# Performance work log

Measured on AMD Instinct MI355X. Metric: run time of the kernel, lower is better.

The kernel has to match this reference:

```python
import jax, jax.numpy as jnp
import numpy as np

N = 128          # number of nodes (particles)
NR = N * (N - 1) # number of directed edges, receiver-major order
B = 128          # batch
C = 16           # channel dim


def setup_inputs() -> dict:
    key = jax.random.key(0)
    x = jax.random.normal(key, (B, NR, C), dtype=jnp.float32)
    # assign_matrices enumerates (r, s) pairs receiver-major, so edge i has
    # receiver i // (N-1); Rr2 is the one-hot indicator of this mapping.
    receivers = jnp.arange(NR, dtype=jnp.int32) // (N - 1)
    return {"x": x, "receivers": receivers}


def reference(x, receivers):
    # exp of edge scores
    e = jnp.exp(x)  # [B, Nr, C]
    # tensordot(exp, Rr2, axes=[1,1]) == segment-sum over edges grouped by receiver
    seg = jax.ops.segment_sum(e.transpose(1, 0, 2), receivers, num_segments=N)  # [N, B, C]
    # tensordot(exp_sum, Rr2, axes=1) == gather each edge's receiver sum back to edges
    denom = seg[receivers]                 # [Nr, B, C]
    denom = denom.transpose(1, 2, 0)       # [B, C, Nr]
    # NOTE: the original divides the raw inputs (not exp) by the summed exp
    return x.transpose(0, 2, 1) / denom    # [B, C, Nr]
```

## Files before the change

kernel.cpp:

```cpp
#include <hip/hip_runtime.h>

#define NN   128
#define NE   127
#define CH   16
#define NRE  (NN * NE)
#define STR  128

__global__ __launch_bounds__(256) void attn2_kernel(const float* __restrict__ x,
                                                    float* __restrict__ out) {
    __shared__ float tile[4][CH * STR];

    const int t   = threadIdx.x & 63;
    const int w   = threadIdx.x >> 6;
    const int seg = (blockIdx.x << 2) | w;
    const int b   = seg >> 7;
    const int r   = seg & (NN - 1);

    float* T = tile[w];

    const float4* xseg = (const float4*)(x + (size_t)seg * NE * CH);

    float4 v[8];
    #pragma unroll
    for (int it = 0; it < 8; ++it) {
        int f = t + (it << 6);
        v[it] = xseg[f < 508 ? f : 507];
    }

    const int p  = (t & 3) << 2;
    const int er = t >> 2;
    float a0 = 0.f, a1 = 0.f, a2 = 0.f, a3 = 0.f;
    #pragma unroll
    for (int it = 0; it < 8; ++it) {
        int f = t + (it << 6);
        if (f < 508) {
            int edge = er + (it << 4);
            T[(p + 0) * STR + edge] = v[it].x;
            T[(p + 1) * STR + edge] = v[it].y;
            T[(p + 2) * STR + edge] = v[it].z;
            T[(p + 3) * STR + edge] = v[it].w;
            a0 += __expf(v[it].x); a1 += __expf(v[it].y);
            a2 += __expf(v[it].z); a3 += __expf(v[it].w);
        }
    }

    #pragma unroll
    for (int m = 4; m <= 32; m <<= 1) {
        a0 += __shfl_xor(a0, m, 64);
        a1 += __shfl_xor(a1, m, 64);
        a2 += __shfl_xor(a2, m, 64);
        a3 += __shfl_xor(a3, m, 64);
    }
    if (t < 4) {
        T[(p + 0) * STR + NE] = 1.0f / a0;
        T[(p + 1) * STR + NE] = 1.0f / a1;
        T[(p + 2) * STR + NE] = 1.0f / a2;
        T[(p + 3) * STR + NE] = 1.0f / a3;
    }
    __syncthreads();

    float* oseg = out + (size_t)b * CH * NRE + (size_t)r * NE;
    #pragma unroll
    for (int c = 0; c < CH; ++c) {
        float rd = T[c * STR + NE];
        float* row = oseg + (size_t)c * NRE;
        row[t] = T[c * STR + t] * rd;
        if (t < 63) row[64 + t] = T[c * STR + 64 + t] * rd;
    }
}

extern "C" void kernel_launch(void* const* d_in, const int* in_sizes, int n_in,
                              void* d_out, int out_size, void* d_ws, size_t ws_size,
                              hipStream_t stream) {
    const float* x = (const float*)d_in[0];
    float* out = (float*)d_out;
    attn2_kernel<<<(128 * 128) / 4, 256, 0, stream>>>(x, out);
}
```

Measured before the change: 238.6 us.

## Process four contiguous receivers per block cooperatively with float4 output stores

Each block now handles a contiguous chunk of 4 receivers (508 edges) cooperatively instead of one receiver per wavefront. Per-receiver sums are split across row boundaries, reduced with shuffles, and combined across waves in shared memory. The output is written as aligned float4 stores over the 508-element contiguous chunk per channel, replacing the scalar 127-wide row writes. This adds an extra sync, a divide by 127 in the store index math, and larger shared memory per block.

New measurement: 235.1 us. About the same (-1.5%).

```diff
diff --git a/kernel.cpp b/kernel.cpp
--- a/kernel.cpp
+++ b/kernel.cpp
@@ -4,68 +4,106 @@
 #define NE   127
 #define CH   16
 #define NRE  (NN * NE)
-#define STR  128
+#define RPB  4
+#define EPB  (RPB * NE)
+#define F4PB (EPB * CH / 4)
 
-__global__ __launch_bounds__(256) void attn2_kernel(const float* __restrict__ x,
-                                                    float* __restrict__ out) {
-    __shared__ float tile[4][CH * STR];
+__global__ __launch_bounds__(256, 4)
+void attn2_kernel(const float* __restrict__ x, float* __restrict__ out) {
+    __shared__ __align__(16) float T[CH][EPB];
+    __shared__ float4 P[4][RPB][4];
+    __shared__ float  R[RPB][CH];
 
-    const int t   = threadIdx.x & 63;
-    const int w   = threadIdx.x >> 6;
-    const int seg = (blockIdx.x << 2) | w;
-    const int b   = seg >> 7;
-    const int r   = seg & (NN - 1);
+    const int tid = threadIdx.x;
+    const int w   = tid >> 6;
+    const int t   = tid & 63;
+    const int cg  = tid & 3;
+    const int e0  = tid >> 2;
 
-    float* T = tile[w];
+    const int b   = blockIdx.x >> 5;
+    const int chk = blockIdx.x & 31;
 
-    const float4* xseg = (const float4*)(x + (size_t)seg * NE * CH);
+    const float4* xs4 = (const float4*)(x + ((size_t)b * NRE + (size_t)chk * EPB) * CH);
 
     float4 v[8];
     #pragma unroll
     for (int it = 0; it < 8; ++it) {
-        int f = t + (it << 6);
-        v[it] = xseg[f < 508 ? f : 507];
+        int f = tid + (it << 8);
+        v[it] = xs4[f < F4PB ? f : F4PB - 1];
     }
 
-    const int p  = (t & 3) << 2;
-    const int er = t >> 2;
-    float a0 = 0.f, a1 = 0.f, a2 = 0.f, a3 = 0.f;
+    float4 acc[RPB];
+    #pragma unroll
+    for (int r = 0; r < RPB; ++r) acc[r] = float4{0.f, 0.f, 0.f, 0.f};
+
+    const int c0 = cg << 2;
     #pragma unroll
     for (int it = 0; it < 8; ++it) {
-        int f = t + (it << 6);
-        if (f < 508) {
-            int edge = er + (it << 4);
-            T[(p + 0) * STR + edge] = v[it].x;
-            T[(p + 1) * STR + edge] = v[it].y;
-            T[(p + 2) * STR + edge] = v[it].z;
-            T[(p + 3) * STR + edge] = v[it].w;
-            a0 += __expf(v[it].x); a1 += __expf(v[it].y);
-            a2 += __expf(v[it].z); a3 += __expf(v[it].w);
+        int f = tid + (it << 8);
+        if (f < F4PB) {
+            int e = e0 + (it << 6);
+            T[c0 + 0][e] = v[it].x;
+            T[c0 + 1][e] = v[it].y;
+            T[c0 + 2][e] = v[it].z;
+            T[c0 + 3][e] = v[it].w;
+            float ex = __expf(v[it].x), ey = __expf(v[it].y);
+            float ez = __expf(v[it].z), ew = __expf(v[it].w);
+            const int m = it >> 1;
+            if ((it & 1) == 0) {
+                acc[m].x += ex; acc[m].y += ey; acc[m].z += ez; acc[m].w += ew;
+            } else if (it == 7) {
+                acc[3].x += ex; acc[3].y += ey; acc[3].z += ez; acc[3].w += ew;
+            } else if (e0 < 63 - m) {
+                acc[m].x += ex; acc[m].y += ey; acc[m].z += ez; acc[m].w += ew;
+            } else {
+                acc[m + 1].x += ex; acc[m + 1].y += ey;
+                acc[m + 1].z += ez; acc[m + 1].w += ew;
+            }
         }
     }
 
     #pragma unroll
-    for (int m = 4; m <= 32; m <<= 1) {
-        a0 += __shfl_xor(a0, m, 64);
-        a1 += __shfl_xor(a1, m, 64);
-        a2 += __shfl_xor(a2, m, 64);
-        a3 += __shfl_xor(a3, m, 64);
+    for (int msk = 4; msk <= 32; msk <<= 1) {
+        #pragma unroll
+        for (int r = 0; r < RPB; ++r) {
+            acc[r].x += __shfl_xor(acc[r].x, msk, 64);
+            acc[r].y += __shfl_xor(acc[r].y, msk, 64);
+            acc[r].z += __shfl_xor(acc[r].z, msk, 64);
+            acc[r].w += __shfl_xor(acc[r].w, msk, 64);
+        }
     }
     if (t < 4) {
-        T[(p + 0) * STR + NE] = 1.0f / a0;
-        T[(p + 1) * STR + NE] = 1.0f / a1;
-        T[(p + 2) * STR + NE] = 1.0f / a2;
-        T[(p + 3) * STR + NE] = 1.0f / a3;
+        #pragma unroll
+        for (int r = 0; r < RPB; ++r) P[w][r][t] = acc[r];
     }
     __syncthreads();
 
-    float* oseg = out + (size_t)b * CH * NRE + (size_t)r * NE;
+    if (tid < 64) {
+        int r = tid >> 4, c = tid & 15, j = c & 3;
+        const float* p0 = (const float*)&P[0][r][c >> 2];
+        const float* p1 = (const float*)&P[1][r][c >> 2];
+        const float* p2 = (const float*)&P[2][r][c >> 2];
+        const float* p3 = (const float*)&P[3][r][c >> 2];
+        R[r][c] = 1.0f / (p0[j] + p1[j] + p2[j] + p3[j]);
+    }
+    __syncthreads();
+
+    float* ob = out + (size_t)b * CH * NRE + (size_t)chk * EPB;
     #pragma unroll
-    for (int c = 0; c < CH; ++c) {
-        float rd = T[c * STR + NE];
-        float* row = oseg + (size_t)c * NRE;
-        row[t] = T[c * STR + t] * rd;
-        if (t < 63) row[64 + t] = T[c * STR + 64 + t] * rd;
+    for (int it = 0; it < 8; ++it) {
+        int f2 = tid + (it << 8);
+        if (f2 < F4PB) {
+            int c = f2 / NE;
+            int m = f2 - c * NE;
+            int e = m << 2;
+            const float4 val = *(const float4*)&T[c][e];
+            float4 o;
+            o.x = val.x * R[(e + 0) / NE][c];
+            o.y = val.y * R[(e + 1) / NE][c];
+            o.z = val.z * R[(e + 2) / NE][c];
+            o.w = val.w * R[(e + 3) / NE][c];
+            *(float4*)(ob + (size_t)c * NRE + e) = o;
+        }
     }
 }
 
@@ -74,5 +112,5 @@
                               hipStream_t stream) {
     const float* x = (const float*)d_in[0];
     float* out = (float*)d_out;
-    attn2_kernel<<<(128 * 128) / 4, 256, 0, stream>>>(x, out);
+    attn2_kernel<<<128 * 32, 256, 0, stream>>>(x, out);
 }
```
